# Kernel optimization log

Hardware: AMD Instinct MI355X
Metric: run time of the kernel (lower is better)

Reference implementation:

```python
import jax, jax.numpy as jnp
import numpy as np

N = 50000          # nodes
E = 800000         # edges
G = 256            # graphs in batch
DIMS = [(64, 16), (16, 32), (32, 64), (64, 64), (64, 128)]  # GCNConv (in,out) per layer


def setup_inputs() -> dict:
    key = jax.random.key(0)
    ks = jax.random.split(key, 16)
    inp = {
        'x': jax.random.normal(ks[0], (N, DIMS[0][0]), dtype=jnp.float32),
        'edge_index': jax.random.randint(ks[1], (2, E), 0, N, dtype=jnp.int64),
        'edge_weight': jax.random.uniform(ks[2], (E,), dtype=jnp.float32),
        'batch': jnp.sort(jax.random.randint(ks[3], (N,), 0, G, dtype=jnp.int64)),
    }
    for i, (fi, fo) in enumerate(DIMS):
        scale = 1.0 / np.sqrt(fi)
        inp[f'W{i+1}'] = jax.random.normal(ks[4 + 2 * i], (fi, fo), dtype=jnp.float32) * scale
        inp[f'b{i+1}'] = jax.random.normal(ks[5 + 2 * i], (fo,), dtype=jnp.float32) * 0.01
    return inp


def gcn_conv(x, src, dst, w, W, b):
    # PyG GCNConv: add self-loops (weight 1), symmetric degree normalization,
    # linear transform, scatter-add aggregation at target nodes, plus bias.
    xw = x @ W                                           # [N, Fout]
    ar = jnp.arange(N, dtype=src.dtype)
    s = jnp.concatenate([src, ar])
    d = jnp.concatenate([dst, ar])
    ww = jnp.concatenate([w, jnp.ones((N,), dtype=w.dtype)])
    deg = jax.ops.segment_sum(ww, d, num_segments=N)     # [N]
    dinv = jnp.where(deg > 0, jax.lax.rsqrt(deg), 0.0)
    norm = dinv[s] * ww * dinv[d]                        # [E+N]
    out = jax.ops.segment_sum(norm[:, None] * xw[s], d, num_segments=N)
    return out + b


def reference(x, edge_index, edge_weight, batch, W1, b1, W2, b2, W3, b3, W4, b4, W5, b5):
    src, dst = edge_index[0], edge_index[1]
    h = jax.nn.relu(gcn_conv(x, src, dst, edge_weight, W1, b1))
    h = jax.nn.relu(gcn_conv(h, src, dst, edge_weight, W2, b2))
    h = jax.nn.relu(gcn_conv(h, src, dst, edge_weight, W3, b3))
    h = jax.nn.relu(gcn_conv(h, src, dst, edge_weight, W4, b4))
    h = gcn_conv(h, src, dst, edge_weight, W5, b5)
    pooled = jax.ops.segment_sum(h, batch, num_segments=G)  # global_add_pool
    return jax.nn.relu(pooled)
```

## Files before the change

kernel.cpp:

```cpp
#include <hip/hip_runtime.h>

#define NN 50000
#define NE 800000
#define NG 256
#define NBUK 782
#define EPB 1563
#define NBLK 512
#define PSLICE 8


__device__ __forceinline__ float bflo(unsigned u) { return __uint_as_float(u << 16); }
__device__ __forceinline__ float bfhi(unsigned u) { return __uint_as_float(u & 0xFFFF0000u); }
__device__ __forceinline__ unsigned bfr_hi(float x) {
    unsigned u = __float_as_uint(x);
    return (u + 0x7FFFu + ((u >> 16) & 1u)) & 0xFFFF0000u;
}
__device__ __forceinline__ unsigned bfpack2(float x, float y) {
    unsigned ux = __float_as_uint(x), uy = __float_as_uint(y);
    unsigned lx = (ux + 0x7FFFu + ((ux >> 16) & 1u)) >> 16;
    unsigned hy = (uy + 0x7FFFu + ((uy >> 16) & 1u)) & 0xFFFF0000u;
    return lx | hy;
}
__device__ __forceinline__ void bfacc8(float* A, float c, uint4 v) {
    A[0] += c * bflo(v.x); A[1] += c * bfhi(v.x);
    A[2] += c * bflo(v.y); A[3] += c * bfhi(v.y);
    A[4] += c * bflo(v.z); A[5] += c * bfhi(v.z);
    A[6] += c * bflo(v.w); A[7] += c * bfhi(v.w);
}


__global__ __launch_bounds__(256) void kA1(const int* __restrict__ dst,
                                           int* __restrict__ pbb) {
    __shared__ int hist[NBUK];
    for (int k = threadIdx.x; k < NBUK; k += 256) hist[k] = 0;
    __syncthreads();
    int b = blockIdx.x;
    int e0 = b * EPB, e1 = min(NE, e0 + EPB);
    for (int i = e0 + threadIdx.x; i < e1; i += 256)
        atomicAdd(&hist[dst[i] >> 6], 1);
    __syncthreads();
    for (int k = threadIdx.x; k < NBUK; k += 256)
        pbb[k * NBLK + b] = hist[k];
}

__global__ __launch_bounds__(256) void k_pbbscan(int* __restrict__ pbb,
                                                 int* __restrict__ bucketCnt) {
    int k = blockIdx.x * 4 + (threadIdx.x >> 6);
    int lane = threadIdx.x & 63;
    if (k >= NBUK) return;
    int* row = pbb + (size_t)k * NBLK;
    int run = 0;
    for (int base = 0; base < NBLK; base += 64) {
        int idx = base + lane;
        int v = (idx < NBLK) ? row[idx] : 0;
        int inc = v;
        for (int off = 1; off < 64; off *= 2) {
            int u = __shfl_up(inc, off);
            if (lane >= off) inc += u;
        }
        if (idx < NBLK) row[idx] = inc - v + run;
        run += __shfl(inc, 63);
    }
    if (lane == 0) bucketCnt[k] = run;
}

__global__ __launch_bounds__(1024) void k_bscan(const int* __restrict__ bucketCnt,
                                                int* __restrict__ bucketBase,
                                                int* __restrict__ rowptr) {
    __shared__ int wsum[16];
    int tid = threadIdx.x;
    int v = (tid < NBUK) ? bucketCnt[tid] : 0;
    int inc = v;
    for (int off = 1; off < 64; off *= 2) {
        int u = __shfl_up(inc, off);
        if ((tid & 63) >= off) inc += u;
    }
    if ((tid & 63) == 63) wsum[tid >> 6] = inc;
    __syncthreads();
    if (tid < 16) {
        int w = wsum[tid], winc = w;
        for (int off = 1; off < 16; off *= 2) {
            int u = __shfl_up(winc, off);
            if (tid >= off) winc += u;
        }
        wsum[tid] = winc - w;
    }
    __syncthreads();
    int ex = inc - v + wsum[tid >> 6];
    if (tid <= NBUK) bucketBase[tid] = ex;
    if (tid == 0) rowptr[NN] = NE;
}

__global__ __launch_bounds__(256) void kA2(const int* __restrict__ src,
                                           const int* __restrict__ dst,
                                           const float* __restrict__ w,
                                           const int* __restrict__ bucketBase,
                                           const int* __restrict__ pbb,
                                           int2* __restrict__ tmp) {
    __shared__ int cur[NBUK];
    __shared__ int base[NBUK];
    int b = blockIdx.x;
    for (int k = threadIdx.x; k < NBUK; k += 256) {
        base[k] = bucketBase[k] + pbb[k * NBLK + b];
        cur[k] = 0;
    }
    __syncthreads();
    int e0 = b * EPB, e1 = min(NE, e0 + EPB);
    for (int i = e0 + threadIdx.x; i < e1; i += 256) {
        int d = dst[i];
        int k = d >> 6;
        int pos = base[k] + atomicAdd(&cur[k], 1);
        tmp[pos] = make_int2(((d & 63) << 16) | src[i], __float_as_int(w[i]));
    }
}

__global__ __launch_bounds__(256) void kB(const int2* __restrict__ tmp,
                                          const int* __restrict__ bucketBase,
                                          int* __restrict__ rowptr,
                                          float* __restrict__ dinv,
                                          float* __restrict__ selfc,
                                          unsigned* __restrict__ sedge) {
    __shared__ int   cnt[64];
    __shared__ float degs[64];
    __shared__ int   curs[64];
    int b = blockIdx.x;
    int tid = threadIdx.x;
    if (tid < 64) { cnt[tid] = 0; degs[tid] = 0.f; }
    __syncthreads();
    int s0 = bucketBase[b], s1 = bucketBase[b + 1];
    for (int p = s0 + tid; p < s1; p += 256) {
        int2 e = tmp[p];
        int n6 = e.x >> 16;
        atomicAdd(&cnt[n6], 1);
        atomicAdd(&degs[n6], __int_as_float(e.y));
    }
    __syncthreads();
    if (tid < 64) {
        int c = cnt[tid];
        int inc = c;
        for (int off = 1; off < 64; off *= 2) {
            int u = __shfl_up(inc, off);
            if (tid >= off) inc += u;
        }
        int ex = inc - c;
        curs[tid] = ex;
        int node = b * 64 + tid;
        if (node < NN) {
            rowptr[node] = s0 + ex;
            float deg = 1.0f + degs[tid];
            float r = rsqrtf(deg);
            dinv[node] = r;
            selfc[node] = r * r;
        }
    }
    __syncthreads();
    for (int p = s0 + tid; p < s1; p += 256) {
        int2 e = tmp[p];
        int n6 = e.x >> 16;
        int pos = s0 + atomicAdd(&curs[n6], 1);
        sedge[pos] = (unsigned)(e.x & 0xFFFF) | bfr_hi(__int_as_float(e.y));
    }
}

__global__ void k_coef(const int* __restrict__ rowptr, const float* __restrict__ dinv,
                       unsigned* __restrict__ sedge) {
    int r = blockIdx.x * blockDim.x + threadIdx.x;
    if (r >= NN) return;
    int e0 = rowptr[r], e1 = rowptr[r + 1];
    float dr = dinv[r];
    for (int p = e0; p < e1; ++p) {
        unsigned u = sedge[p];
        float c = dinv[u & 0xFFFFu] * bfhi(u) * dr;
        sedge[p] = (u & 0xFFFFu) | bfr_hi(c);
    }
}


template<int G>
__device__ __forceinline__ void agg_row_bf(const uint4* __restrict__ h4,
                                           const unsigned* __restrict__ se,
                                           int lane, int e0, int e1, float* acc) {
    float b0[8], b1[8], b2[8];
    #pragma unroll
    for (int j = 0; j < 8; ++j) { b0[j] = 0.f; b1[j] = 0.f; b2[j] = 0.f; }
    int p = e0;
    for (; p + 4 <= e1; p += 4) {
        unsigned u0 = se[p], u1 = se[p + 1], u2 = se[p + 2], u3 = se[p + 3];
        uint4 v0 = h4[(long long)(u0 & 0xFFFFu) * G + lane];
        uint4 v1 = h4[(long long)(u1 & 0xFFFFu) * G + lane];
        uint4 v2 = h4[(long long)(u2 & 0xFFFFu) * G + lane];
        uint4 v3 = h4[(long long)(u3 & 0xFFFFu) * G + lane];
        bfacc8(acc, bfhi(u0), v0);
        bfacc8(b0,  bfhi(u1), v1);
        bfacc8(b1,  bfhi(u2), v2);
        bfacc8(b2,  bfhi(u3), v3);
    }
    for (; p < e1; ++p) {
        unsigned u = se[p];
        uint4 v = h4[(long long)(u & 0xFFFFu) * G + lane];
        bfacc8(acc, bfhi(u), v);
    }
    #pragma unroll
    for (int j = 0; j < 8; ++j) acc[j] += (b0[j] + b1[j]) + b2[j];
}


template<int F, bool BRELU>
__global__ void k_agg_bf(const unsigned* __restrict__ h, const int* __restrict__ rowptr,
                         const unsigned* __restrict__ se, const float* __restrict__ selfc,
                         const float* __restrict__ bias, unsigned* __restrict__ out, int n) {
    constexpr int G = F / 8;
    constexpr int NPB = 256 / G;
    int gid = blockIdx.x * NPB + threadIdx.x / G;
    int lane = threadIdx.x & (G - 1);
    if (gid >= n) return;
    const uint4* h4 = (const uint4*)h;
    float acc[8];
    #pragma unroll
    for (int j = 0; j < 8; ++j) acc[j] = 0.f;
    uint4 sv = h4[(long long)gid * G + lane];
    bfacc8(acc, selfc[gid], sv);
    agg_row_bf<G>(h4, se, lane, rowptr[gid], rowptr[gid + 1], acc);
    if (BRELU) {
        float4 bv0 = ((const float4*)bias)[lane * 2];
        float4 bv1 = ((const float4*)bias)[lane * 2 + 1];
        acc[0] = fmaxf(acc[0] + bv0.x, 0.f); acc[1] = fmaxf(acc[1] + bv0.y, 0.f);
        acc[2] = fmaxf(acc[2] + bv0.z, 0.f); acc[3] = fmaxf(acc[3] + bv0.w, 0.f);
        acc[4] = fmaxf(acc[4] + bv1.x, 0.f); acc[5] = fmaxf(acc[5] + bv1.y, 0.f);
        acc[6] = fmaxf(acc[6] + bv1.z, 0.f); acc[7] = fmaxf(acc[7] + bv1.w, 0.f);
    }
    uint4 o;
    o.x = bfpack2(acc[0], acc[1]); o.y = bfpack2(acc[2], acc[3]);
    o.z = bfpack2(acc[4], acc[5]); o.w = bfpack2(acc[6], acc[7]);
    ((uint4*)out)[(long long)gid * G + lane] = o;
}


template<int FAGG, int FOUT, int ROWS, bool RELU>
__global__ __launch_bounds__(256) void k_aggemm_bf(const unsigned* __restrict__ h,
                                                   const int* __restrict__ rowptr,
                                                   const unsigned* __restrict__ se,
                                                   const float* __restrict__ selfc,
                                                   const float* __restrict__ W,
                                                   const float* __restrict__ b,
                                                   unsigned* __restrict__ out, int n) {
    constexpr int G    = FAGG / 8;
    constexpr int NPP  = 256 / G;
    constexpr int PASS = ROWS / NPP;
    constexpr int SA   = ROWS + 4;
    constexpr int TC   = FOUT / 4;
    constexpr int TR   = 256 / TC;
    constexpr int R    = ROWS / TR;

    __shared__ float  hT[FAGG * SA];
    __shared__ float4 bl[TC];

    int tid = threadIdx.x;
    int rowbase = blockIdx.x * ROWS;
    const float4* Wf4 = (const float4*)W;

    if (tid < TC) bl[tid] = ((const float4*)b)[tid];

    const uint4* h4 = (const uint4*)h;
    int lane = tid & (G - 1);
    int sub  = tid / G;
    #pragma unroll
    for (int ps = 0; ps < PASS; ++ps) {
        int lrow = ps * NPP + sub;
        int gid = rowbase + lrow;
        int gidc = (gid < n) ? gid : (n - 1);
        float acc[8];
        #pragma unroll
        for (int j = 0; j < 8; ++j) acc[j] = 0.f;
        uint4 sv = h4[(long long)gidc * G + lane];
        bfacc8(acc, selfc[gidc], sv);
        agg_row_bf<G>(h4, se, lane, rowptr[gidc], rowptr[gidc + 1], acc);
        #pragma unroll
        for (int j = 0; j < 8; ++j)
            hT[(8 * lane + j) * SA + lrow] = acc[j];
    }
    __syncthreads();

    int tc = tid % TC;
    int r0 = (tid / TC) * R;

    float4 acc[R];
    float4 binit = bl[tc];
    #pragma unroll
    for (int r = 0; r < R; ++r) acc[r] = binit;

    #pragma unroll 4
    for (int fi = 0; fi < FAGG; ++fi) {
        float4 wv = __ldg(&Wf4[fi * TC + tc]);
        float a[R];
        if constexpr (R >= 4) {
            #pragma unroll
            for (int rb = 0; rb < R / 4; ++rb) {
                float4 t = *(const float4*)&hT[fi * SA + r0 + 4 * rb];
                a[4 * rb + 0] = t.x; a[4 * rb + 1] = t.y;
                a[4 * rb + 2] = t.z; a[4 * rb + 3] = t.w;
            }
        } else if constexpr (R == 2) {
            float2 t = *(const float2*)&hT[fi * SA + r0];
            a[0] = t.x; a[1] = t.y;
        } else {
            a[0] = hT[fi * SA + r0];
        }
        #pragma unroll
        for (int r = 0; r < R; ++r) {
            acc[r].x += a[r] * wv.x; acc[r].y += a[r] * wv.y;
            acc[r].z += a[r] * wv.z; acc[r].w += a[r] * wv.w;
        }
    }

    #pragma unroll
    for (int r = 0; r < R; ++r) {
        int row = rowbase + r0 + r;
        if (row < n) {
            float4 v = acc[r];
            if (RELU) {
                v.x = fmaxf(v.x, 0.f); v.y = fmaxf(v.y, 0.f);
                v.z = fmaxf(v.z, 0.f); v.w = fmaxf(v.w, 0.f);
            }
            uint2 o;
            o.x = bfpack2(v.x, v.y); o.y = bfpack2(v.z, v.w);
            ((uint2*)out)[(long long)row * (FOUT / 4) + tc] = o;
        }
    }
}


template<int FIN, int FOUT, bool RELU, bool BIAS>
__global__ __launch_bounds__(256) void k_gemm_bf(const float* __restrict__ h,
                                                 const float* __restrict__ W,
                                                 const float* __restrict__ b,
                                                 unsigned* __restrict__ out, int n) {
    constexpr int TC = FOUT / 4;
    constexpr int TR = 256 / TC;
    constexpr int R  = 64 / TR;
    constexpr int SA = 68;
    constexpr int CB = FIN / 4;

    __shared__ float  hT[FIN * SA];
    __shared__ float4 Wl[FIN * TC];
    __shared__ float4 bl[TC];

    int tid = threadIdx.x;
    int rowbase = blockIdx.x * 64;

    for (int i = tid; i < FIN * TC; i += 256) Wl[i] = ((const float4*)W)[i];
    if (BIAS && tid < TC) bl[tid] = ((const float4*)b)[tid];

    for (int blk = tid; blk < 16 * CB; blk += 256) {
        int br = blk / CB, bc = blk % CB;
        float4 v[4];
        #pragma unroll
        for (int i = 0; i < 4; ++i) {
            int rr = rowbase + 4 * br + i;
            if (rr >= n) rr = n - 1;
            v[i] = *(const float4*)(h + (long long)rr * FIN + 4 * bc);
        }
        #pragma unroll
        for (int j = 0; j < 4; ++j) {
            float4 t;
            t.x = ((float*)&v[0])[j];
            t.y = ((float*)&v[1])[j];
            t.z = ((float*)&v[2])[j];
            t.w = ((float*)&v[3])[j];
            *(float4*)&hT[(4 * bc + j) * SA + 4 * br] = t;
        }
    }
    __syncthreads();

    int tc = tid % TC;
    int r0 = (tid / TC) * R;

    float4 acc[R];
    float4 binit = BIAS ? bl[tc] : make_float4(0.f, 0.f, 0.f, 0.f);
    #pragma unroll
    for (int r = 0; r < R; ++r) acc[r] = binit;

    #pragma unroll 4
    for (int fi = 0; fi < FIN; ++fi) {
        float4 wv = Wl[fi * TC + tc];
        float a[R];
        if constexpr (R >= 4) {
            #pragma unroll
            for (int rb = 0; rb < R / 4; ++rb) {
                float4 t = *(const float4*)&hT[fi * SA + r0 + 4 * rb];
                a[4 * rb + 0] = t.x; a[4 * rb + 1] = t.y;
                a[4 * rb + 2] = t.z; a[4 * rb + 3] = t.w;
            }
        } else if constexpr (R == 2) {
            float2 t = *(const float2*)&hT[fi * SA + r0];
            a[0] = t.x; a[1] = t.y;
        } else {
            a[0] = hT[fi * SA + r0];
        }
        #pragma unroll
        for (int r = 0; r < R; ++r) {
            acc[r].x += a[r] * wv.x; acc[r].y += a[r] * wv.y;
            acc[r].z += a[r] * wv.z; acc[r].w += a[r] * wv.w;
        }
    }

    #pragma unroll
    for (int r = 0; r < R; ++r) {
        int row = rowbase + r0 + r;
        if (row < n) {
            float4 v = acc[r];
            if (RELU) {
                v.x = fmaxf(v.x, 0.f); v.y = fmaxf(v.y, 0.f);
                v.z = fmaxf(v.z, 0.f); v.w = fmaxf(v.w, 0.f);
            }
            uint2 o;
            o.x = bfpack2(v.x, v.y); o.y = bfpack2(v.z, v.w);
            ((uint2*)out)[(long long)row * (FOUT / 4) + tc] = o;
        }
    }
}


__global__ __launch_bounds__(64) void k_pool1(const unsigned* __restrict__ h,
                                              const int* __restrict__ batch,
                                              float* __restrict__ part, int n) {
    int g = blockIdx.x / PSLICE;
    int s = blockIdx.x % PSLICE;
    int lo = 0, hi = n;
    while (lo < hi) { int m = (lo + hi) >> 1; if (batch[m] < g) lo = m + 1; else hi = m; }
    int start = lo;
    hi = n;
    while (lo < hi) { int m = (lo + hi) >> 1; if (batch[m] < g + 1) lo = m + 1; else hi = m; }
    int end = lo;
    int len = end - start;
    int a = start + (int)((long long)len * s / PSLICE);
    int bnd = start + (int)((long long)len * (s + 1) / PSLICE);
    int t = threadIdx.x;
    float a0 = 0.f, a1 = 0.f, b0 = 0.f, b1 = 0.f;
    int i = a;
    for (; i + 2 <= bnd; i += 2) {
        unsigned u0 = h[(long long)(i + 0) * 64 + t];
        unsigned u1 = h[(long long)(i + 1) * 64 + t];
        a0 += bflo(u0); a1 += bfhi(u0);
        b0 += bflo(u1); b1 += bfhi(u1);
    }
    if (i < bnd) {
        unsigned u0 = h[(long long)i * 64 + t];
        a0 += bflo(u0); a1 += bfhi(u0);
    }
    part[(long long)blockIdx.x * 128 + 2 * t]     = a0 + b0;
    part[(long long)blockIdx.x * 128 + 2 * t + 1] = a1 + b1;
}

__global__ __launch_bounds__(128) void k_pool2(const float* __restrict__ part,
                                               float* __restrict__ out) {
    int g = blockIdx.x;
    int f = threadIdx.x;
    float acc = 0.f;
    #pragma unroll
    for (int s = 0; s < PSLICE; ++s)
        acc += part[(long long)(g * PSLICE + s) * 128 + f];
    out[g * 128 + f] = fmaxf(acc, 0.0f);
}


static inline int cdiv(long long a, int b) { return (int)((a + b - 1) / b); }

extern "C" void kernel_launch(void* const* d_in, const int* in_sizes, int n_in,
                              void* d_out, int out_size, void* d_ws, size_t ws_size,
                              hipStream_t stream) {
    const float* x    = (const float*)d_in[0];
    const int*   src  = (const int*)d_in[1];
    const int*   dst  = src + NE;
    const float* ew   = (const float*)d_in[2];
    const int*   batch= (const int*)d_in[3];
    const float* W1 = (const float*)d_in[4];  const float* b1 = (const float*)d_in[5];
    const float* W2 = (const float*)d_in[6];  const float* b2 = (const float*)d_in[7];
    const float* W3 = (const float*)d_in[8];  const float* b3 = (const float*)d_in[9];
    const float* W4 = (const float*)d_in[10]; const float* b4 = (const float*)d_in[11];
    const float* W5 = (const float*)d_in[12]; const float* b5 = (const float*)d_in[13];
    float* out = (float*)d_out;

    float* ws = (float*)d_ws;
    int*      rowptr = (int*)ws;
    unsigned* sedge  = (unsigned*)(ws + 50004);
    float*    selfc  = ws + 50004 + 2 * (size_t)NE;
    float*    dinv   = selfc + NN;
    float*    bufA   = dinv + NN;
    float*    bufB   = bufA + (size_t)NN * 64;
    unsigned* hA  = (unsigned*)bufA;
    unsigned* hB  = (unsigned*)bufB;
    int*  pbb        = (int*)bufA;
    int*  bucketCnt  = pbb + NBUK * NBLK;
    int*  bucketBase = bucketCnt + NBUK + 1;
    int2* tmp        = (int2*)bufB;
    float* part      = bufA + (size_t)NN * 32;

    const int T = 256;

    kA1<<<NBLK, T, 0, stream>>>(dst, pbb);
    k_pbbscan<<<cdiv(NBUK, 4), T, 0, stream>>>(pbb, bucketCnt);
    k_bscan<<<1, 1024, 0, stream>>>(bucketCnt, bucketBase, rowptr);
    kA2<<<NBLK, T, 0, stream>>>(src, dst, ew, bucketBase, pbb, tmp);
    kB<<<NBUK, T, 0, stream>>>(tmp, bucketBase, rowptr, dinv, selfc, sedge);
    k_coef<<<cdiv(NN, T), T, 0, stream>>>(rowptr, dinv, sedge);

    k_gemm_bf<64, 16, false, false><<<cdiv(NN, 64), T, 0, stream>>>(x, W1, nullptr, hA, NN);
    k_agg_bf<16, true><<<cdiv(NN, 128), T, 0, stream>>>(hA, rowptr, sedge, selfc, b1, hB, NN);

    k_aggemm_bf<16, 32, 128, true ><<<cdiv(NN, 128), T, 0, stream>>>(hB, rowptr, sedge, selfc, W2, b2, hA, NN);
    k_aggemm_bf<32, 64,  64, true ><<<cdiv(NN, 64),  T, 0, stream>>>(hA, rowptr, sedge, selfc, W3, b3, hB, NN);
    k_aggemm_bf<64, 64,  64, true ><<<cdiv(NN, 64),  T, 0, stream>>>(hB, rowptr, sedge, selfc, W4, b4, hA, NN);
    k_aggemm_bf<64, 128, 64, false><<<cdiv(NN, 64),  T, 0, stream>>>(hA, rowptr, sedge, selfc, W5, b5, hB, NN);

    k_pool1<<<NG * PSLICE, 64, 0, stream>>>(hB, batch, part, NN);
    k_pool2<<<NG, 128, 0, stream>>>(part, out);
}
```

Baseline: 179.0 us.

## Coarsen CSR-build buckets to 256 nodes and merge scans into one kernel

```diff
diff --git a/kernel.cpp b/kernel.cpp
--- a/kernel.cpp
+++ b/kernel.cpp
@@ -3,9 +3,9 @@
 #define NN 50000
 #define NE 800000
 #define NG 256
-#define NBUK 782
-#define EPB 1563
-#define NBLK 512
+#define NBUK 196
+#define EPB 3125
+#define NBLK 256
 #define PSLICE 8
 
 
@@ -37,58 +37,35 @@
     int b = blockIdx.x;
     int e0 = b * EPB, e1 = min(NE, e0 + EPB);
     for (int i = e0 + threadIdx.x; i < e1; i += 256)
-        atomicAdd(&hist[dst[i] >> 6], 1);
+        atomicAdd(&hist[dst[i] >> 8], 1);
     __syncthreads();
     for (int k = threadIdx.x; k < NBUK; k += 256)
-        pbb[k * NBLK + b] = hist[k];
-}
-
-__global__ __launch_bounds__(256) void k_pbbscan(int* __restrict__ pbb,
-                                                 int* __restrict__ bucketCnt) {
-    int k = blockIdx.x * 4 + (threadIdx.x >> 6);
-    int lane = threadIdx.x & 63;
-    if (k >= NBUK) return;
-    int* row = pbb + (size_t)k * NBLK;
+        pbb[b * NBUK + k] = hist[k];
+}
+
+__global__ __launch_bounds__(256) void k_scan(int* __restrict__ pbb,
+                                              int* __restrict__ bucketBase,
+                                              int* __restrict__ rowptr) {
+    int t = threadIdx.x;
     int run = 0;
-    for (int base = 0; base < NBLK; base += 64) {
-        int idx = base + lane;
-        int v = (idx < NBLK) ? row[idx] : 0;
-        int inc = v;
-        for (int off = 1; off < 64; off *= 2) {
-            int u = __shfl_up(inc, off);
-            if (lane >= off) inc += u;
-        }
-        if (idx < NBLK) row[idx] = inc - v + run;
-        run += __shfl(inc, 63);
-    }
-    if (lane == 0) bucketCnt[k] = run;
-}
-
-__global__ __launch_bounds__(1024) void k_bscan(const int* __restrict__ bucketCnt,
-                                                int* __restrict__ bucketBase,
-                                                int* __restrict__ rowptr) {
-    __shared__ int wsum[16];
-    int tid = threadIdx.x;
-    int v = (tid < NBUK) ? bucketCnt[tid] : 0;
-    int inc = v;
+    for (int b = 0; b < NBLK; ++b) {
+        int v = (t < NBUK) ? pbb[b * NBUK + t] : 0;
+        if (t < NBUK) pbb[b * NBUK + t] = run;
+        run += v;
+    }
+    __shared__ int wsum[4];
+    int inc = run;
     for (int off = 1; off < 64; off *= 2) {
         int u = __shfl_up(inc, off);
-        if ((tid & 63) >= off) inc += u;
-    }
-    if ((tid & 63) == 63) wsum[tid >> 6] = inc;
-    __syncthreads();
-    if (tid < 16) {
-        int w = wsum[tid], winc = w;
-        for (int off = 1; off < 16; off *= 2) {
-            int u = __shfl_up(winc, off);
-            if (tid >= off) winc += u;
-        }
-        wsum[tid] = winc - w;
-    }
-    __syncthreads();
-    int ex = inc - v + wsum[tid >> 6];
-    if (tid <= NBUK) bucketBase[tid] = ex;
-    if (tid == 0) rowptr[NN] = NE;
+        if ((t & 63) >= off) inc += u;
+    }
+    if ((t & 63) == 63) wsum[t >> 6] = inc;
+    __syncthreads();
+    if (t == 0) { int s = 0; for (int i = 0; i < 4; ++i) { int x = wsum[i]; wsum[i] = s; s += x; } }
+    __syncthreads();
+    int ex = inc - run + wsum[t >> 6];
+    if (t < NBUK) bucketBase[t] = ex;
+    if (t == 0) { bucketBase[NBUK] = NE; rowptr[NN] = NE; }
 }
 
 __global__ __launch_bounds__(256) void kA2(const int* __restrict__ src,
@@ -101,16 +78,16 @@
     __shared__ int base[NBUK];
     int b = blockIdx.x;
     for (int k = threadIdx.x; k < NBUK; k += 256) {
-        base[k] = bucketBase[k] + pbb[k * NBLK + b];
+        base[k] = bucketBase[k] + pbb[b * NBUK + k];
         cur[k] = 0;
     }
     __syncthreads();
     int e0 = b * EPB, e1 = min(NE, e0 + EPB);
     for (int i = e0 + threadIdx.x; i < e1; i += 256) {
         int d = dst[i];
-        int k = d >> 6;
+        int k = d >> 8;
         int pos = base[k] + atomicAdd(&cur[k], 1);
-        tmp[pos] = make_int2(((d & 63) << 16) | src[i], __float_as_int(w[i]));
+        tmp[pos] = make_int2(((d & 255) << 16) | src[i], __float_as_int(w[i]));
     }
 }
 
@@ -120,44 +97,47 @@
                                           float* __restrict__ dinv,
                                           float* __restrict__ selfc,
                                           unsigned* __restrict__ sedge) {
-    __shared__ int   cnt[64];
-    __shared__ float degs[64];
-    __shared__ int   curs[64];
+    __shared__ int   cnt[256];
+    __shared__ float degs[256];
+    __shared__ int   curs[256];
+    __shared__ int   wsum[4];
     int b = blockIdx.x;
     int tid = threadIdx.x;
-    if (tid < 64) { cnt[tid] = 0; degs[tid] = 0.f; }
+    cnt[tid] = 0; degs[tid] = 0.f;
     __syncthreads();
     int s0 = bucketBase[b], s1 = bucketBase[b + 1];
     for (int p = s0 + tid; p < s1; p += 256) {
         int2 e = tmp[p];
-        int n6 = e.x >> 16;
-        atomicAdd(&cnt[n6], 1);
-        atomicAdd(&degs[n6], __int_as_float(e.y));
-    }
-    __syncthreads();
-    if (tid < 64) {
-        int c = cnt[tid];
-        int inc = c;
-        for (int off = 1; off < 64; off *= 2) {
-            int u = __shfl_up(inc, off);
-            if (tid >= off) inc += u;
-        }
-        int ex = inc - c;
-        curs[tid] = ex;
-        int node = b * 64 + tid;
-        if (node < NN) {
-            rowptr[node] = s0 + ex;
-            float deg = 1.0f + degs[tid];
-            float r = rsqrtf(deg);
-            dinv[node] = r;
-            selfc[node] = r * r;
-        }
+        int n8 = e.x >> 16;
+        atomicAdd(&cnt[n8], 1);
+        atomicAdd(&degs[n8], __int_as_float(e.y));
+    }
+    __syncthreads();
+    int c = cnt[tid];
+    int inc = c;
+    for (int off = 1; off < 64; off *= 2) {
+        int u = __shfl_up(inc, off);
+        if ((tid & 63) >= off) inc += u;
+    }
+    if ((tid & 63) == 63) wsum[tid >> 6] = inc;
+    __syncthreads();
+    if (tid == 0) { int s = 0; for (int i = 0; i < 4; ++i) { int x = wsum[i]; wsum[i] = s; s += x; } }
+    __syncthreads();
+    int ex = inc - c + wsum[tid >> 6];
+    curs[tid] = ex;
+    int node = b * 256 + tid;
+    if (node < NN) {
+        rowptr[node] = s0 + ex;
+        float deg = 1.0f + degs[tid];
+        float r = rsqrtf(deg);
+        dinv[node] = r;
+        selfc[node] = r * r;
     }
     __syncthreads();
     for (int p = s0 + tid; p < s1; p += 256) {
         int2 e = tmp[p];
-        int n6 = e.x >> 16;
-        int pos = s0 + atomicAdd(&curs[n6], 1);
+        int n8 = e.x >> 16;
+        int pos = s0 + atomicAdd(&curs[n8], 1);
         sedge[pos] = (unsigned)(e.x & 0xFFFF) | bfr_hi(__int_as_float(e.y));
     }
 }
@@ -491,16 +471,14 @@
     unsigned* hA  = (unsigned*)bufA;
     unsigned* hB  = (unsigned*)bufB;
     int*  pbb        = (int*)bufA;
-    int*  bucketCnt  = pbb + NBUK * NBLK;
-    int*  bucketBase = bucketCnt + NBUK + 1;
+    int*  bucketBase = pbb + NBLK * NBUK;
     int2* tmp        = (int2*)bufB;
     float* part      = bufA + (size_t)NN * 32;
 
     const int T = 256;
 
     kA1<<<NBLK, T, 0, stream>>>(dst, pbb);
-    k_pbbscan<<<cdiv(NBUK, 4), T, 0, stream>>>(pbb, bucketCnt);
-    k_bscan<<<1, 1024, 0, stream>>>(bucketCnt, bucketBase, rowptr);
+    k_scan<<<1, T, 0, stream>>>(pbb, bucketBase, rowptr);
     kA2<<<NBLK, T, 0, stream>>>(src, dst, ew, bucketBase, pbb, tmp);
     kB<<<NBUK, T, 0, stream>>>(tmp, bucketBase, rowptr, dinv, selfc, sedge);
     k_coef<<<cdiv(NN, T), T, 0, stream>>>(rowptr, dinv, sedge);
```

Result: slower. 218.3 us (+21.9%).
